# Kernel optimization log

Measured on AMD Instinct MI355X. Metric: run time of the kernel, lower is better.

Reference implementation:

```python
import jax, jax.numpy as jnp
from jax import lax
import numpy as np

B, S, IN = 8, 4096, 64
D, H, K = 512, 8, 3
TCN_CH = [256, 256, 512]
HD = D // H


def setup_inputs() -> dict:
    key = jax.random.key(0)
    ks = iter(jax.random.split(key, 64))
    def nrm(shape, s=0.02):
        return jax.random.normal(next(ks), shape, jnp.float32) * s
    inp = {"x": jax.random.normal(next(ks), (B, S, IN), jnp.float32)}
    inp["W_in"] = nrm((IN, D)); inp["b_in"] = jnp.zeros((D,), jnp.float32)
    chans = [D] + TCN_CH
    for i in range(3):
        cin, cout = chans[i], chans[i + 1]
        inp[f"c1w{i}"] = nrm((cout, cin, K), 0.01); inp[f"c1b{i}"] = jnp.zeros((cout,), jnp.float32)
        inp[f"c2w{i}"] = nrm((cout, cout, K), 0.01); inp[f"c2b{i}"] = jnp.zeros((cout,), jnp.float32)
        if cin != cout:  # downsample 1x1 conv (blocks 0 and 2)
            inp[f"dsw{i}"] = nrm((cout, cin, 1), 0.01); inp[f"dsb{i}"] = jnp.zeros((cout,), jnp.float32)
    inp["W_tcn"] = nrm((TCN_CH[-1], D)); inp["b_tcn"] = jnp.zeros((D,), jnp.float32)
    NL = 2  # attention layers, stacked on leading axis
    for n in ["Wq", "Wk", "Wv", "Wo"]:
        inp[n] = nrm((NL, D, D))
    for n in ["bq", "bk", "bv", "bo", "ln_b"]:
        inp[n] = jnp.zeros((NL, D), jnp.float32)
    inp["ln_g"] = jnp.ones((NL, D), jnp.float32)
    inp["W_out"] = nrm((D, 1)); inp["b_out"] = jnp.zeros((1,), jnp.float32)
    return inp


def _conv(x, w, b, dil, pad):
    # x: (B,C,L), w: (O,I,K)
    y = lax.conv_general_dilated(x, w, (1,), [(pad, pad)], rhs_dilation=(dil,),
                                 dimension_numbers=("NCH", "OIH", "NCH"))
    return y + b[None, :, None]


def _block(t, c1w, c1b, c2w, c2b, ds, dil):
    # TemporalConvBlock: symmetric padding (k-1)*dil on both convs, truncate to input length
    pad = (K - 1) * dil
    o = jax.nn.relu(_conv(t, c1w, c1b, dil, pad))   # length L + pad
    o = _conv(o, c2w, c2b, dil, pad)                # length L + 2*pad
    r = t if ds is None else _conv(t, ds[0], ds[1], 1, 0)
    return jax.nn.relu(o[:, :, : t.shape[2]] + r)


def _layernorm(x, g, b, eps=1e-5):
    mu = x.mean(-1, keepdims=True)
    var = ((x - mu) ** 2).mean(-1, keepdims=True)
    return (x - mu) * lax.rsqrt(var + eps) * g + b


def _forward(x, W_in, b_in, c1w0, c1b0, c2w0, c2b0, dsw0, dsb0,
             c1w1, c1b1, c2w1, c2b1, c1w2, c1b2, c2w2, c2b2, dsw2, dsb2,
             W_tcn, b_tcn, Wq, bq, Wk, bk, Wv, bv, Wo, bo, ln_g, ln_b, W_out, b_out):
    h = x @ W_in + b_in                              # (B,S,D)
    t = jnp.swapaxes(h, 1, 2)                        # (B,D,S)
    t = _block(t, c1w0, c1b0, c2w0, c2b0, (dsw0, dsb0), 1)
    t = _block(t, c1w1, c1b1, c2w1, c2b1, None, 2)
    t = _block(t, c1w2, c1b2, c2w2, c2b2, (dsw2, dsb2), 4)
    h = h + jnp.swapaxes(t, 1, 2) @ W_tcn + b_tcn
    # sinusoidal positional encoding
    pos = jnp.arange(S, dtype=jnp.float32)[:, None]
    div = jnp.exp(jnp.arange(0, D, 2, dtype=jnp.float32) * (-np.log(10000.0) / D))
    pe = jnp.stack([jnp.sin(pos * div), jnp.cos(pos * div)], axis=-1).reshape(S, D)
    h = h + pe[None]
    for l in range(Wq.shape[0]):
        res = h
        def heads(y):  # (B,S,D) -> (B,H,S,HD)
            return y.reshape(B, S, H, HD).transpose(0, 2, 1, 3)
        q = heads(h @ Wq[l] + bq[l])
        k = heads(h @ Wk[l] + bk[l])
        v = heads(h @ Wv[l] + bv[l])
        qf = jax.nn.elu(q) + 1.0
        kf = jax.nn.elu(k) + 1.0
        kv = jnp.einsum("bhnd,bhnm->bhdm", kf, v)            # (B,H,HD,HD)
        out = jnp.einsum("bhnd,bhdm->bhnm", qf, kv)          # (B,H,S,HD)
        norm = jnp.maximum(jnp.einsum("bhnd,bhd->bhn", qf, kf.sum(2)), 1e-6)
        out = out / norm[..., None]
        out = out.transpose(0, 2, 1, 3).reshape(B, S, D)
        h = _layernorm(res + out @ Wo[l] + bo[l], ln_g[l], ln_b[l])
    pooled = h.mean(1)                                       # (B,D)
    return (pooled @ W_out + b_out)[:, 0]                    # (B,)


def reference(x, W_in, b_in, c1w0, c1b0, c2w0, c2b0, dsw0, dsb0,
              c1w1, c1b1, c2w1, c2b1, c1w2, c1b2, c2w2, c2b2, dsw2, dsb2,
              W_tcn, b_tcn, Wq, bq, Wk, bk, Wv, bv, Wo, bo, ln_g, ln_b, W_out, b_out):
    return _forward(x, W_in, b_in, c1w0, c1b0, c2w0, c2b0, dsw0, dsb0,
                    c1w1, c1b1, c2w1, c2b1, c1w2, c1b2, c2w2, c2b2, dsw2, dsb2,
                    W_tcn, b_tcn, Wq, bq, Wk, bk, Wv, bv, Wo, bo, ln_g, ln_b, W_out, b_out)
```

## Files before the change

kernel.cpp:

```cpp
#include <hip/hip_runtime.h>

typedef unsigned short u16;
typedef unsigned int u32;
typedef short bhalf8 __attribute__((ext_vector_type(8)));
typedef float f32x4 __attribute__((ext_vector_type(4)));

#define S_LEN 4096
#define NSEG 30

__device__ __forceinline__ float b2f(u16 h){ return __uint_as_float(((u32)h) << 16); }
__device__ __forceinline__ u16 f2b(float f){
  u32 u = __float_as_uint(f);
  return (u16)((u + 0x7FFFu + ((u >> 16) & 1u)) >> 16);
}
__device__ __forceinline__ u32 cvtpk(float a, float b){
  u32 r; asm("v_cvt_pk_bf16_f32 %0, %1, %2" : "=v"(r) : "v"(a), "v"(b)); return r;
}
__device__ __forceinline__ void unp8(uint4 v, float* f){
  f[0]=__uint_as_float(v.x<<16); f[1]=__uint_as_float(v.x&0xffff0000u);
  f[2]=__uint_as_float(v.y<<16); f[3]=__uint_as_float(v.y&0xffff0000u);
  f[4]=__uint_as_float(v.z<<16); f[5]=__uint_as_float(v.z&0xffff0000u);
  f[6]=__uint_as_float(v.w<<16); f[7]=__uint_as_float(v.w&0xffff0000u);
}
__device__ __forceinline__ void unp4(uint2 v, float* f){
  f[0]=__uint_as_float(v.x<<16); f[1]=__uint_as_float(v.x&0xffff0000u);
  f[2]=__uint_as_float(v.y<<16); f[3]=__uint_as_float(v.y&0xffff0000u);
}

__device__ __forceinline__ size_t taddr(int r, int c, int C){
  return (size_t)(r >> 7) * ((size_t)C << 7) + (size_t)((c >> 5) << 12)
       + ((r & 127) << 5) + (c & 31);
}

__device__ __forceinline__ void gload16(const void* g, void* l){
  __builtin_amdgcn_global_load_lds(
      (__attribute__((address_space(1))) void*)(g),
      (__attribute__((address_space(3))) void*)(l), 16, 0, 0);
}

struct PrepArgs {
  const float* src[NSEG];
  int N[NSEG]; int K[NSEG]; int sn[NSEG]; int sk[NSEG]; unsigned off[NSEG];
};

__global__ __launch_bounds__(256) void prep_w(PrepArgs pa, u16* __restrict__ wb){
  int seg = blockIdx.y;
  int N = pa.N[seg], K = pa.K[seg];
  int ntk = (K + 31) >> 5;
  int tiles = ((N + 31) >> 5) * ntk;
  int tile = blockIdx.x;
  if (tile >= tiles) return;
  int n0 = (tile / ntk) << 5, k0 = (tile % ntk) << 5;
  const float* src = pa.src[seg];
  long sn = pa.sn[seg], sk = pa.sk[seg];
  u16* dst = wb + pa.off[seg];
  int lk = threadIdx.x & 31, ln = threadIdx.x >> 5;
  #pragma unroll
  for (int i = 0; i < 4; ++i){
    int n = n0 + ln + i*8, k = k0 + lk;
    if (n < N && k < K)
      dst[(size_t)n*K + k] = f2b(src[(long)n*sn + (long)k*sk]);
  }
}

__global__ __launch_bounds__(256) void pe_k(float* __restrict__ pe){
  int id = blockIdx.x*256 + threadIdx.x;
  int s = id >> 8, i = id & 255;
  float div = expf((float)i * (-2.0f * 9.210340371976184f / 512.0f));
  float a = (float)s * div;
  pe[(size_t)s*512 + 2*i]   = sinf(a);
  pe[(size_t)s*512 + 2*i+1] = cosf(a);
}

__global__ __launch_bounds__(256) void cvt_k(const float* __restrict__ x, u16* __restrict__ xb, int n){
  int id = blockIdx.x*256 + threadIdx.x;
  if (id < n){
    int r = id >> 6, c = id & 63;
    xb[taddr(r, c, 64)] = f2b(x[id]);
  }
}

template<int KTOT>
__global__ __launch_bounds__(512, 1) void gemm8_k(
    const u16* __restrict__ A, const u16* __restrict__ W,
    const float* __restrict__ bias, const float* __restrict__ bias2,
    const float* __restrict__ bias3,
    u16* __restrict__ out, const u16* __restrict__ resb,
    const float* __restrict__ peb,
    int N, int nN, int flags)
{
  constexpr int KT = KTOT >> 6;
  constexpr int IT = KT >> 1;
  __shared__ u16 As[2][16384];
  __shared__ u16 Bs[2][16384];
  const int tid = threadIdx.x;
  const int wave = tid >> 6, lane = tid & 63;
  const int wm = wave >> 2, wn = wave & 3;
  const int c0 = lane >> 4, fro = lane & 15;

  const int nwg = gridDim.x;
  const int lin = blockIdx.x;
  const int swz = (lin & 7) * (nwg >> 3) + (lin >> 3);
  const int mb = swz / nN, nb = swz - mb * nN;
  const int m0 = mb << 8, n0 = nb << 8;

  const f32x4 zf = {0.f,0.f,0.f,0.f};
  f32x4 acc[8][4];
  #pragma unroll
  for (int i=0;i<8;++i)
    #pragma unroll
    for (int j=0;j<4;++j) acc[i][j] = zf;

  bhalf8 af[2][2], bf[4][2];

  auto SA = [&](int t, int q){
    int s = (q << 9) + tid;
    int row = s >> 3, phys = s & 7;
    int lc = phys ^ (row & 7);
    int grow = m0 + row;
    int gcol = (t << 6) + (lc << 3);
    size_t ga = ((size_t)(grow >> 7) << 16) + (size_t)((gcol >> 5) << 12)
              + ((grow & 127) << 5) + (gcol & 31);
    gload16(A + ga, &As[t & 1][(q << 12) + (wave << 9)]);
  };
  auto SB = [&](int t, int j){
    int s = (j << 9) + tid;
    int row = s >> 3, phys = s & 7;
    int lc = phys ^ (row & 7);
    gload16(W + (size_t)(n0 + row) * KTOT + (t << 6) + (lc << 3),
            &Bs[t & 1][(j << 12) + (wave << 9)]);
  };
  auto LDB = [&](int t){
    #pragma unroll
    for (int nt=0;nt<4;++nt)
      #pragma unroll
      for (int ks=0;ks<2;++ks){
        int row = (wn << 6) + (nt << 4) + fro;
        int phys = ((ks << 2) + c0) ^ (row & 7);
        bf[nt][ks] = *(const bhalf8*)&Bs[t & 1][(row << 6) + (phys << 3)];
      }
  };
  auto LDA = [&](int t, int q){
    #pragma unroll
    for (int mtl=0;mtl<2;++mtl)
      #pragma unroll
      for (int ks=0;ks<2;++ks){
        int row = (q << 6) + (wm << 5) + (mtl << 4) + fro;
        int phys = ((ks << 2) + c0) ^ (row & 7);
        af[mtl][ks] = *(const bhalf8*)&As[t & 1][(row << 6) + (phys << 3)];
      }
  };
  auto BAR = [&]{
    __builtin_amdgcn_sched_barrier(0);
    __builtin_amdgcn_s_barrier();
    __builtin_amdgcn_sched_barrier(0);
  };
  auto MM = [&](int q){
    __builtin_amdgcn_s_setprio(1);
    #pragma unroll
    for (int mtl=0;mtl<2;++mtl)
      #pragma unroll
      for (int nt=0;nt<4;++nt){
        acc[(q<<1)+mtl][nt] = __builtin_amdgcn_mfma_f32_16x16x32_bf16(
            bf[nt][0], af[mtl][0], acc[(q<<1)+mtl][nt], 0, 0, 0);
        acc[(q<<1)+mtl][nt] = __builtin_amdgcn_mfma_f32_16x16x32_bf16(
            bf[nt][1], af[mtl][1], acc[(q<<1)+mtl][nt], 0, 0, 0);
      }
    __builtin_amdgcn_s_setprio(0);
  };

  #pragma unroll
  for (int x=0;x<4;++x){ SA(0,x); SB(0,x); }
  #pragma unroll
  for (int x=0;x<3;++x){ SA(1,x); SB(1,x); }
  asm volatile("s_waitcnt vmcnt(6)" ::: "memory");
  BAR();

  #pragma unroll
  for (int i=0;i<IT;++i){
    const int t0 = 2*i, t1 = 2*i+1, t2 = 2*i+2, t3 = 2*i+3;
    #pragma unroll
    for (int q=0;q<4;++q){
      if (q == 0) LDB(t0);
      LDA(t0, q);
      if (q == 0){ SA(t1,3); SB(t1,3); }
      else if (t2 < KT){ SA(t2,q-1); SB(t2,q-1); }
      BAR();
      MM(q);
      if (q == 3){
        if (t2 < KT) asm volatile("s_waitcnt vmcnt(6)" ::: "memory");
        else         asm volatile("s_waitcnt vmcnt(0)" ::: "memory");
      }
      BAR();
    }
    #pragma unroll
    for (int q=0;q<4;++q){
      if (q == 0) LDB(t1);
      LDA(t1, q);
      if (q == 0){ if (t2 < KT){ SA(t2,3); SB(t2,3); } }
      else if (t3 < KT){ SA(t3,q-1); SB(t3,q-1); }
      BAR();
      MM(q);
      if (q == 3 && (i + 1 < IT))
        asm volatile("s_waitcnt vmcnt(6)" ::: "memory");
      BAR();
    }
  }

  const int th = n0 >> 9;
  #pragma unroll
  for (int mt = 0; mt < 8; ++mt){
    const int row = m0 + ((mt >> 1) << 6) + (wm << 5) + ((mt & 1) << 4) + fro;
    const size_t prow = (size_t)(row & (S_LEN - 1)) * 512;
    #pragma unroll
    for (int nt = 0; nt < 4; ++nt){
      const int col = n0 + (wn << 6) + (nt << 4) + (c0 << 2);
      float v0 = acc[mt][nt][0], v1 = acc[mt][nt][1], v2 = acc[mt][nt][2], v3 = acc[mt][nt][3];
      if (flags & 32){
        const float* bp = (th == 0) ? bias : ((th == 1) ? bias2 : bias3);
        if (bp){ float4 b4 = *(const float4*)&bp[col & 511]; v0+=b4.x; v1+=b4.y; v2+=b4.z; v3+=b4.w; }
      } else {
        if (bias){ float4 b4 = *(const float4*)&bias[col]; v0+=b4.x; v1+=b4.y; v2+=b4.z; v3+=b4.w; }
      }
      if (flags & 4){
        uint2 rv = *(const uint2*)(resb + taddr(row, col, N));
        float rf[4]; unp4(rv, rf);
        v0 += rf[0]; v1 += rf[1]; v2 += rf[2]; v3 += rf[3];
      }
      if (flags & 8){
        float4 p4 = *(const float4*)&peb[prow + col];
        v0 += p4.x; v1 += p4.y; v2 += p4.z; v3 += p4.w;
      }
      if (flags & 1){
        v0 = fmaxf(v0, 0.f); v1 = fmaxf(v1, 0.f); v2 = fmaxf(v2, 0.f); v3 = fmaxf(v3, 0.f);
      }
      if ((flags & 2) && (!(flags & 32) || th < 2)){
        v0 = (v0 > 0.f) ? (v0 + 1.f) : __expf(v0);
        v1 = (v1 > 0.f) ? (v1 + 1.f) : __expf(v1);
        v2 = (v2 > 0.f) ? (v2 + 1.f) : __expf(v2);
        v3 = (v3 > 0.f) ? (v3 + 1.f) : __expf(v3);
      }
      uint2 pk; pk.x = cvtpk(v0, v1); pk.y = cvtpk(v2, v3);
      *(uint2*)(out + taddr(row, col, N)) = pk;
    }
  }
}

template<int NTAPS, int KS1, int KS2>
__global__ __launch_bounds__(256) void gemm_k(
    const u16* __restrict__ A, const u16* __restrict__ W,
    const u16* __restrict__ A2, const u16* __restrict__ W2,
    const float* __restrict__ bias, const float* __restrict__ bias2,
    const float* __restrict__ bias3,
    u16* __restrict__ out, const u16* __restrict__ resb,
    const float* __restrict__ peb, const float* __restrict__ den,
    int N, int CA, int CA2, int dil, int nN, int wbstride, int flags)
{
  constexpr bool MT   = (NTAPS == 3);
  constexpr int HALO  = MT ? 8 : 0;
  constexpr int AR    = MT ? 144 : 128;
  constexpr int DA    = MT ? ((KS2 > 0) ? 3 : 2) : 3;
  constexpr int DB    = 3;
  constexpr int K     = KS1 << 5;
  constexpr int K2    = KS2 << 5;
  constexpr int TOTAL = MT ? (3*KS1 + KS2) : (KS1 + KS2);
  __shared__ u16 As[DA][AR*32];
  __shared__ u16 Bs[DB][128*32];
  const int tid = threadIdx.x;
  const int wave = tid >> 6, lane = tid & 63;
  const int wm = wave >> 1, wn = wave & 1;

  const int nwg = gridDim.x;
  const int lin = blockIdx.x;
  const int swz = (lin & 7) * (nwg >> 3) + (lin >> 3);
  const int mb = swz / nN, nb = swz - mb * nN;
  const int m0 = mb << 7, n0 = nb << 7;
  const bool bnd = (m0 & (S_LEN - 1)) == 0;

  const u16* Ae = (flags & 16) ? (A + (((size_t)(n0 & 511) >> 5) << 12)) : A;

  const int lr4 = lane >> 2, lc4 = lane & 3;
  const int c0 = lane >> 4, fro = lane & 15;

  const f32x4 zf = {0.f, 0.f, 0.f, 0.f};
  const bhalf8 zb = {0,0,0,0,0,0,0,0};
  f32x4 acc[4][4];
  #pragma unroll
  for (int i=0;i<4;++i)
    #pragma unroll
    for (int j=0;j<4;++j) acc[i][j] = zf;

  const u16* Wb = W + (size_t)(m0 >> 12) * (size_t)wbstride;
  const size_t abase  = (size_t)mb * ((size_t)CA  << 7);
  const size_t abase2 = (size_t)mb * ((size_t)CA2 << 7);

  auto STAGE_A = [&](int kb, int ab){
    const size_t tb = abase + ((size_t)kb << 12);
    #pragma unroll
    for (int half = 0; half < 2; ++half){
      int mrow = (wave << 5) + (half << 4) + lr4;
      int i = mrow + HALO;
      int cg = lc4 ^ ((i >> 1) & 3);
      gload16(Ae + tb + mrow*32 + (cg << 3), &As[ab][(HALO + (wave << 5) + (half << 4)) * 32]);
    }
    if (MT && wave == 0 && lane < 32){
      int j = lr4;
      int cg = lc4 ^ ((j >> 1) & 3);
      size_t hb_ = (mb ? abase - ((size_t)CA << 7) : abase) + ((size_t)kb << 12) + (120 + j)*32;
      gload16(Ae + hb_ + (cg << 3), &As[ab][0]);
    }
  };
  auto STAGE_A2 = [&](int t2, int ab){
    const size_t tb = abase2 + ((size_t)t2 << 12);
    #pragma unroll
    for (int half = 0; half < 2; ++half){
      int mrow = (wave << 5) + (half << 4) + lr4;
      int i = mrow + HALO;
      int cg = lc4 ^ ((i >> 1) & 3);
      gload16(A2 + tb + mrow*32 + (cg << 3), &As[ab][(HALO + (wave << 5) + (half << 4)) * 32]);
    }
  };
  auto STAGE_B = [&](const u16* Wt, size_t kstride, int kb, int bb){
    #pragma unroll
    for (int half = 0; half < 2; ++half){
      int i = (wave << 5) + (half << 4) + lr4;
      int cg = lc4 ^ ((i >> 1) & 3);
      gload16(Wt + (size_t)(n0 + i) * kstride + (kb << 5) + (cg << 3),
              &Bs[bb][((wave << 5) + (half << 4)) * 32]);
    }
  };
  auto DO16 = [&](int ab, int bb, int sh, bool mask){
    bhalf8 af[4], bf[4];
    #pragma unroll
    for (int mt = 0; mt < 4; ++mt){
      int r8 = (wm << 6) + (mt << 4) + fro + HALO + sh;
      af[mt] = *(const bhalf8*)&As[ab][r8 * 32 + ((c0 ^ ((r8 >> 1) & 3)) << 3)];
    }
    if (MT && mask && bnd && wm == 0 && fro + sh < 0) af[0] = zb;
    #pragma unroll
    for (int nt = 0; nt < 4; ++nt){
      int rB = (wn << 6) + (nt << 4) + fro;
      bf[nt] = *(const bhalf8*)&Bs[bb][rB * 32 + ((c0 ^ ((rB >> 1) & 3)) << 3)];
    }
    #pragma unroll
    for (int mt = 0; mt < 4; ++mt)
      #pragma unroll
      for (int nt = 0; nt < 4; ++nt)
        acc[mt][nt] = __builtin_amdgcn_mfma_f32_16x16x32_bf16(bf[nt], af[mt], acc[mt][nt], 0, 0, 0);
  };

  if constexpr (!MT){
    auto STG = [&](int s){
      int b = s % 3;
      if (s < KS1){ STAGE_A(s, b); STAGE_B(Wb, (size_t)K, s, b); }
      else if (KS2 > 0){ STAGE_A2(s - KS1, b); STAGE_B(W2, (size_t)K2, s - KS1, b); }
    };
    STG(0);
    if constexpr (TOTAL > 1) STG(1);
    #pragma unroll
    for (int s = 0; s < TOTAL; ++s){
      if (s + 1 >= TOTAL) asm volatile("s_waitcnt vmcnt(0)" ::: "memory");
      else                asm volatile("s_waitcnt vmcnt(4)" ::: "memory");
      __builtin_amdgcn_sched_barrier(0);
      __builtin_amdgcn_s_barrier();
      __builtin_amdgcn_sched_barrier(0);
      if (s + 2 < TOTAL) STG(s + 2);
      DO16(s % 3, s % 3, 0, false);
    }
  } else {
    auto STG = [&](int s){
      if (s < 3*KS1){
        int kb = s / 3, tap = s % 3;
        if (tap == 0) STAGE_A(kb, kb % DA);
        STAGE_B(Wb + (size_t)tap * N * K, (size_t)K, kb, s % 3);
      } else if (KS2 > 0){
        int t2 = s - 3*KS1;
        STAGE_A2(t2, (KS1 + t2) % DA);
        STAGE_B(W2, (size_t)K2, t2, s % 3);
      }
    };
    STG(0);
    if constexpr (TOTAL > 1) STG(1);
    #pragma unroll
    for (int s = 0; s < TOTAL; ++s){
      if (s + 1 >= TOTAL) asm volatile("s_waitcnt vmcnt(0)" ::: "memory");
      else                asm volatile("s_waitcnt vmcnt(2)" ::: "memory");
      __builtin_amdgcn_sched_barrier(0);
      __builtin_amdgcn_s_barrier();
      __builtin_amdgcn_sched_barrier(0);
      if (s + 2 < TOTAL) STG(s + 2);
      if (s < 3*KS1) DO16((s/3) % DA, s % 3, ((s%3) - 2) * dil, true);
      else           DO16((KS1 + (s - 3*KS1)) % DA, s % 3, 0, false);
    }
  }

  const int mb_l = (wm << 6) + fro;
  const int cb_l = (wn << 6) + (c0 << 2);
  const int th = n0 >> 9;
  #pragma unroll
  for (int mt = 0; mt < 4; ++mt){
    const int row = m0 + mb_l + (mt << 4);
    const size_t prow = (size_t)(row & (S_LEN - 1)) * 512;
    #pragma unroll
    for (int nt = 0; nt < 4; ++nt){
      const int col = n0 + cb_l + (nt << 4);
      float v0 = acc[mt][nt][0], v1 = acc[mt][nt][1], v2 = acc[mt][nt][2], v3 = acc[mt][nt][3];
      if (flags & 32){
        const float* bp = (th == 0) ? bias : ((th == 1) ? bias2 : bias3);
        if (bp){ float4 b4 = *(const float4*)&bp[col & 511]; v0+=b4.x; v1+=b4.y; v2+=b4.z; v3+=b4.w; }
      } else {
        if (bias) { float4 b4 = *(const float4*)&bias[col];  v0+=b4.x; v1+=b4.y; v2+=b4.z; v3+=b4.w; }
        if (bias2){ float4 b4 = *(const float4*)&bias2[col]; v0+=b4.x; v1+=b4.y; v2+=b4.z; v3+=b4.w; }
      }
      if (flags & 4){
        uint2 rv = *(const uint2*)(resb + taddr(row, col, N));
        float rf[4]; unp4(rv, rf);
        v0 += rf[0]; v1 += rf[1]; v2 += rf[2]; v3 += rf[3];
      }
      if (flags & 8){
        float4 p4 = *(const float4*)&peb[prow + col];
        v0 += p4.x; v1 += p4.y; v2 += p4.z; v3 += p4.w;
      }
      if (flags & 16){
        float d = fmaxf(den[((size_t)row << 3) + (col >> 6)], 1e-6f);
        float rd = 1.0f / d;
        v0 *= rd; v1 *= rd; v2 *= rd; v3 *= rd;
      }
      if (flags & 1){
        v0 = fmaxf(v0, 0.f); v1 = fmaxf(v1, 0.f); v2 = fmaxf(v2, 0.f); v3 = fmaxf(v3, 0.f);
      }
      if ((flags & 2) && (!(flags & 32) || th < 2)){
        v0 = (v0 > 0.f) ? (v0 + 1.f) : __expf(v0);
        v1 = (v1 > 0.f) ? (v1 + 1.f) : __expf(v1);
        v2 = (v2 > 0.f) ? (v2 + 1.f) : __expf(v2);
        v3 = (v3 > 0.f) ? (v3 + 1.f) : __expf(v3);
      }
      uint2 pk; pk.x = cvtpk(v0, v1); pk.y = cvtpk(v2, v3);
      *(uint2*)(out + taddr(row, col, N)) = pk;
    }
  }
}

__global__ __launch_bounds__(256) void kv_partial(
    const u16* __restrict__ qkv,
    float* __restrict__ kvp, float* __restrict__ ksp)
{
  const int bh = blockIdx.x;
  const int b = bh >> 3, h = bh & 7;
  const int ch = blockIdx.y;
  const int t = threadIdx.x;
  __shared__ u16 kfs[16][64];
  __shared__ u16 vs[16][64];
  float acc[4][4] = {{0.f}};
  float ks[4] = {0.f,0.f,0.f,0.f};
  const int d0 = (t >> 4) << 2;
  const int c0 = (t & 15) << 2;
  const int lr = t >> 4, lc = (t & 15) << 2;
  const int rowbase = (b << 12) + (ch << 9);
  const int ck = 512 + (h << 6) + lc;
  const int cv = 1024 + (h << 6) + lc;
  for (int g = 0; g < 32; ++g){
    int r = rowbase + (g << 4) + lr;
    *(uint2*)&kfs[lr][lc] = *(const uint2*)(qkv + taddr(r, ck, 1536));
    *(uint2*)&vs[lr][lc]  = *(const uint2*)(qkv + taddr(r, cv, 1536));
    __syncthreads();
    #pragma unroll
    for (int i = 0; i < 16; ++i){
      float kv4[4], vv4[4];
      unp4(*(const uint2*)&kfs[i][d0], kv4);
      unp4(*(const uint2*)&vs[i][c0], vv4);
      #pragma unroll
      for (int j=0;j<4;++j)
        #pragma unroll
        for (int k2=0;k2<4;++k2) acc[j][k2] += kv4[j]*vv4[k2];
      if ((t & 15) == 0){
        #pragma unroll
        for (int j=0;j<4;++j) ks[j] += kv4[j];
      }
    }
    __syncthreads();
  }
  float* dst = kvp + ((size_t)(bh << 3) + ch) * 4096;
  #pragma unroll
  for (int j=0;j<4;++j)
    #pragma unroll
    for (int k2=0;k2<4;++k2) dst[(d0+j)*64 + (c0+k2)] = acc[j][k2];
  if ((t & 15) == 0){
    float* kd = ksp + ((size_t)(bh << 3) + ch) * 64;
    #pragma unroll
    for (int j=0;j<4;++j) kd[d0+j] = ks[j];
  }
}

__global__ __launch_bounds__(256) void kvred_k(
    const float* __restrict__ kvp, const float* __restrict__ ksp,
    float* __restrict__ kvf, float* __restrict__ ksf)
{
  int bh = blockIdx.x, t = threadIdx.x;
  for (int e = t; e < 4096; e += 256){
    float s = 0.f;
    #pragma unroll
    for (int ch = 0; ch < 8; ++ch) s += kvp[((size_t)(bh<<3)+ch)*4096 + e];
    kvf[(size_t)bh*4096 + e] = s;
  }
  if (t < 64){
    float s = 0.f;
    #pragma unroll
    for (int ch = 0; ch < 8; ++ch) s += ksp[((size_t)(bh<<3)+ch)*64 + t];
    ksf[bh*64 + t] = s;
  }
}

__global__ __launch_bounds__(256) void denpack_k(const u16* __restrict__ qkv,
    const float* __restrict__ ksf, float* __restrict__ den,
    const float* __restrict__ kvf, u16* __restrict__ wbd)
{
  int bid = blockIdx.x;
  if (bid < 1024){
    int id = bid*256 + threadIdx.x;
    int r = id >> 3, h = id & 7;
    int b = r >> 12;
    const float* ks = ksf + ((b<<3)+h)*64;
    float s = 0.f;
    for (int d = 0; d < 64; d += 8){
      uint4 vq = *(const uint4*)(qkv + taddr(r, (h << 6) + d, 1536));
      float f[8]; unp8(vq, f);
      #pragma unroll
      for (int j=0;j<8;++j) s += f[j]*ks[d+j];
    }
    den[id] = s;
  } else {
    int id = (bid - 1024)*256 + threadIdx.x;
    int b = id >> 16;
    int n = (id >> 7) & 511, j = id & 127;
    float v = 0.f;
    if ((j >> 6) == ((n >> 6) & 1))
      v = kvf[((size_t)((b<<3)+(n>>6)))*4096 + (j & 63)*64 + (n & 63)];
    wbd[id] = f2b(v);
  }
}

__global__ __launch_bounds__(256) void ln_k(const u16* __restrict__ in,
    const float* __restrict__ g, const float* __restrict__ beta, u16* __restrict__ out)
{
  int wave = threadIdx.x >> 6, lane = threadIdx.x & 63;
  int row = blockIdx.x*4 + wave;
  size_t ad = taddr(row, lane*8, 512);
  uint4 pv = *(const uint4*)(in + ad);
  float f[8]; unp8(pv, f);
  float s = 0.f, ss = 0.f;
  #pragma unroll
  for (int i=0;i<8;++i){ s += f[i]; ss += f[i]*f[i]; }
  for (int m=1;m<64;m<<=1){ s += __shfl_xor(s,m); ss += __shfl_xor(ss,m); }
  float mean = s * (1.f/512.f);
  float var = ss * (1.f/512.f) - mean*mean;
  float rstd = rsqrtf(fmaxf(var, 0.f) + 1e-5f);
  u16 o[8];
  #pragma unroll
  for (int i=0;i<8;++i){
    int c = lane*8 + i;
    o[i] = f2b((f[i]-mean)*rstd*g[c] + beta[c]);
  }
  *(uint4*)(out + ad) = *(uint4*)o;
}

__global__ __launch_bounds__(256) void pool1_k(const u16* __restrict__ hb,
    const float* __restrict__ wout, const float* __restrict__ g,
    const float* __restrict__ beta, float* __restrict__ part)
{
  int b = blockIdx.x >> 6, ch = blockIdx.x & 63;
  int t = threadIdx.x;
  __shared__ float ws[512];
  __shared__ float red[256];
  __shared__ float S2[2];
  float a0 = 0.f, a1 = 0.f;
  for (int i = t; i < 512; i += 256){
    float w = wout[i];
    float gw = w * g[i];
    ws[i] = gw;
    a0 += gw;
    a1 += w * beta[i];
  }
  red[t] = a0; __syncthreads();
  for (int k2=128;k2;k2>>=1){ if (t<k2) red[t]+=red[t+k2]; __syncthreads(); }
  if (!t) S2[0] = red[0];
  __syncthreads();
  red[t] = a1; __syncthreads();
  for (int k2=128;k2;k2>>=1){ if (t<k2) red[t]+=red[t+k2]; __syncthreads(); }
  if (!t) S2[1] = red[0];
  __syncthreads();
  const float Sgw = S2[0], Sbw = S2[1];

  int r = (b << 12) + (ch << 6) + (t >> 2);
  int c0 = (t & 3) << 7;
  float sd = 0.f, s1 = 0.f, s2 = 0.f;
  for (int i = 0; i < 128; i += 8){
    uint4 v = *(const uint4*)(hb + taddr(r, c0 + i, 512));
    float f[8]; unp8(v, f);
    #pragma unroll
    for (int j=0;j<8;++j){ float x = f[j]; sd += x*ws[c0+i+j]; s1 += x; s2 += x*x; }
  }
  sd += __shfl_xor(sd,1); s1 += __shfl_xor(s1,1); s2 += __shfl_xor(s2,1);
  sd += __shfl_xor(sd,2); s1 += __shfl_xor(s1,2); s2 += __shfl_xor(s2,2);
  float mean = s1 * (1.f/512.f);
  float var  = s2 * (1.f/512.f) - mean*mean;
  float rstd = rsqrtf(fmaxf(var, 0.f) + 1e-5f);
  float rowv = rstd * (sd - mean * Sgw) + Sbw;
  red[t] = ((t & 3) == 0) ? rowv : 0.f;
  __syncthreads();
  for (int k2=128;k2;k2>>=1){ if (t<k2) red[t]+=red[t+k2]; __syncthreads(); }
  if (!t) part[blockIdx.x] = red[0];
}

__global__ __launch_bounds__(64) void pool2_k(const float* __restrict__ part,
    const float* __restrict__ bout, float* __restrict__ out)
{
  int b = blockIdx.x, t = threadIdx.x;
  float s = part[(b << 6) + t];
  for (int m=1;m<64;m<<=1) s += __shfl_xor(s,m);
  if (!t) out[b] = s * (1.f/4096.f) + bout[0];
}

extern "C" void kernel_launch(void* const* d_in, const int* in_sizes, int n_in,
                              void* d_out, int out_size, void* d_ws, size_t ws_size,
                              hipStream_t stream)
{
  (void)in_sizes; (void)n_in; (void)out_size; (void)ws_size;
  const float* x    = (const float*)d_in[0];
  const float* W_in = (const float*)d_in[1];
  const float* b_in = (const float*)d_in[2];
  const float* c1w0 = (const float*)d_in[3];
  const float* c1b0 = (const float*)d_in[4];
  const float* c2w0 = (const float*)d_in[5];
  const float* c2b0 = (const float*)d_in[6];
  const float* dsw0 = (const float*)d_in[7];
  const float* dsb0 = (const float*)d_in[8];
  const float* c1w1 = (const float*)d_in[9];
  const float* c1b1 = (const float*)d_in[10];
  const float* c2w1 = (const float*)d_in[11];
  const float* c2b1 = (const float*)d_in[12];
  const float* c1w2 = (const float*)d_in[13];
  const float* c1b2 = (const float*)d_in[14];
  const float* c2w2 = (const float*)d_in[15];
  const float* c2b2 = (const float*)d_in[16];
  const float* dsw2 = (const float*)d_in[17];
  const float* dsb2 = (const float*)d_in[18];
  const float* W_tcn= (const float*)d_in[19];
  const float* b_tcn= (const float*)d_in[20];
  const float* Wq   = (const float*)d_in[21];
  const float* Wk   = (const float*)d_in[22];
  const float* Wv   = (const float*)d_in[23];
  const float* Wo   = (const float*)d_in[24];
  const float* bq   = (const float*)d_in[25];
  const float* bk   = (const float*)d_in[26];
  const float* bv   = (const float*)d_in[27];
  const float* bo   = (const float*)d_in[28];
  const float* lnb  = (const float*)d_in[29];
  const float* lng  = (const float*)d_in[30];
  const float* W_out= (const float*)d_in[31];
  const float* b_out= (const float*)d_in[32];

  char* base = (char*)d_ws;
  size_t off = 0;
  auto alloc = [&](size_t bytes) -> void* {
    void* p = base + off;
    off += (bytes + 255) & ~(size_t)255;
    return p;
  };
  u16* WB   = (u16*)alloc(4816896ull*2);
  u16* wbd  = (u16*)alloc(8ull*512*128*2);
  float* peb= (float*)alloc(4096ull*512*4);
  float* den= (float*)alloc(32768ull*8*4);
  float* kvp= (float*)alloc(512ull*4096*4);
  float* ksp= (float*)alloc(512ull*64*4);
  float* kvf= (float*)alloc(64ull*4096*4);
  float* ksf= (float*)alloc(64ull*64*4);
  float* part=(float*)alloc(512*4);
  u16* hb   = (u16*)alloc(32768ull*512*2);
  char* qkvR= (char*)alloc(32768ull*1536*2);
  u16* atto = (u16*)alloc(32768ull*512*2);

  u16* qkvb = (u16*)qkvR;
  u16* xb   = (u16*)(qkvR);
  u16* t1b  = (u16*)(qkvR + 4194304);
  u16* t2b  = (u16*)(qkvR + 20971520);
  u16* t3b  = (u16*)(qkvR + 37748736);
  u16* o1b  = atto;

  unsigned wo_ = 0;
  auto wseg = [&](unsigned e){ unsigned o = wo_; wo_ += e; return o; };
  unsigned oWin  = wseg(512*64);
  unsigned oC1w0 = wseg(3*256*512);
  unsigned oC2w0 = wseg(3*256*256);
  unsigned oDs0  = wseg(256*512);
  unsigned oC1w1 = wseg(3*256*256);
  unsigned oC2w1 = wseg(3*256*256);
  unsigned oC1w2 = wseg(3*512*256);
  unsigned oC2w2 = wseg(3*512*512);
  unsigned oDs2  = wseg(512*256);
  unsigned oWtcn = wseg(512*512);
  unsigned oQKV  = wseg(2*1536*512);
  unsigned oWo   = wseg(2*512*512);

  PrepArgs pa;
  int si = 0;
  auto seg = [&](const float* s, int N, int K, int sn, int sk, unsigned o){
    pa.src[si]=s; pa.N[si]=N; pa.K[si]=K; pa.sn[si]=sn; pa.sk[si]=sk; pa.off[si]=o; ++si;
  };
  seg(W_in, 512, 64, 1, 512, oWin);
  for (int t=0;t<3;++t) seg(c1w0 + t, 256, 512, 1536, 3, oC1w0 + t*131072);
  for (int t=0;t<3;++t) seg(c2w0 + t, 256, 256,  768, 3, oC2w0 + t*65536);
  seg(dsw0, 256, 512, 512, 1, oDs0);
  for (int t=0;t<3;++t) seg(c1w1 + t, 256, 256,  768, 3, oC1w1 + t*65536);
  for (int t=0;t<3;++t) seg(c2w1 + t, 256, 256,  768, 3, oC2w1 + t*65536);
  for (int t=0;t<3;++t) seg(c1w2 + t, 512, 256,  768, 3, oC1w2 + t*131072);
  for (int t=0;t<3;++t) seg(c2w2 + t, 512, 512, 1536, 3, oC2w2 + t*262144);
  seg(dsw2, 512, 256, 256, 1, oDs2);
  seg(W_tcn, 512, 512, 1, 512, oWtcn);
  for (int l=0;l<2;++l){
    seg(Wq + l*262144, 512, 512, 1, 512, oQKV + l*786432 + 0);
    seg(Wk + l*262144, 512, 512, 1, 512, oQKV + l*786432 + 262144);
    seg(Wv + l*262144, 512, 512, 1, 512, oQKV + l*786432 + 524288);
  }
  for (int l=0;l<2;++l) seg(Wo + l*262144, 512, 512, 1, 512, oWo + l*262144);

  prep_w<<<dim3(256, NSEG), 256, 0, stream>>>(pa, WB);
  pe_k<<<4096, 256, 0, stream>>>(peb);
  cvt_k<<<8192, 256, 0, stream>>>(x, xb, 32768*64);

  const int RELU=1, ELU1=2, RES=4, PE=8, DIV=16, QKV=32;
  auto gemm = [&](const u16* A, const u16* W, const u16* A2, const u16* W2,
                  const float* b1, const float* b2, const float* b3,
                  u16* out, const u16* resb,
                  int K, int K2, int N, int CA, int CA2, int ntaps,
                  int dil, int wbs, int flags){
    int nN = N >> 7;
    dim3 grid(256 * nN);
    if (ntaps == 3){
      if (K == 512 && K2 == 0)
        gemm_k<3,16,0><<<grid, 256, 0, stream>>>(A, W, A2, W2, b1, b2, b3, out, resb,
                                                 peb, den, N, CA, CA2, dil, nN, wbs, flags);
      else if (K == 256 && K2 == 512)
        gemm_k<3,8,16><<<grid, 256, 0, stream>>>(A, W, A2, W2, b1, b2, b3, out, resb,
                                                 peb, den, N, CA, CA2, dil, nN, wbs, flags);
      else if (K == 256 && K2 == 0)
        gemm_k<3,8,0><<<grid, 256, 0, stream>>>(A, W, A2, W2, b1, b2, b3, out, resb,
                                                peb, den, N, CA, CA2, dil, nN, wbs, flags);
      else
        gemm_k<3,16,8><<<grid, 256, 0, stream>>>(A, W, A2, W2, b1, b2, b3, out, resb,
                                                 peb, den, N, CA, CA2, dil, nN, wbs, flags);
    } else {
      if (K == 64)
        gemm_k<1,2,0><<<grid, 256, 0, stream>>>(A, W, A2, W2, b1, b2, b3, out, resb,
                                                peb, den, N, CA, CA2, dil, nN, wbs, flags);
      else
        gemm_k<1,4,0><<<grid, 256, 0, stream>>>(A, W, A2, W2, b1, b2, b3, out, resb,
                                                peb, den, N, CA, CA2, dil, nN, wbs, flags);
    }
  };
  auto gemm8 = [&](const u16* A, const u16* W, const float* b1, const float* b2,
                   const float* b3, u16* out, const u16* resb, int N, int flags){
    int nN = N >> 8;
    gemm8_k<512><<<dim3(128 * nN), 512, 0, stream>>>(A, W, b1, b2, b3, out, resb,
                                                     peb, N, nN, flags);
  };

  gemm(xb, WB + oWin, nullptr, nullptr, b_in, nullptr, nullptr, hb, nullptr,
       64, 0, 512, 64, 0, 1, 1, 0, 0);
  gemm(hb,  WB + oC1w0, nullptr, nullptr, c1b0, nullptr, nullptr, o1b, nullptr,
       512, 0, 256, 512, 0, 3, 1, 0, RELU);
  gemm(o1b, WB + oC2w0, hb, WB + oDs0, c2b0, dsb0, nullptr, t1b, nullptr,
       256, 512, 256, 256, 512, 3, 1, 0, RELU);
  gemm(t1b, WB + oC1w1, nullptr, nullptr, c1b1, nullptr, nullptr, o1b, nullptr,
       256, 0, 256, 256, 0, 3, 2, 0, RELU);
  gemm(o1b, WB + oC2w1, nullptr, nullptr, c2b1, nullptr, nullptr, t2b, t1b,
       256, 0, 256, 256, 0, 3, 2, 0, RELU|RES);
  gemm(t2b, WB + oC1w2, nullptr, nullptr, c1b2, nullptr, nullptr, o1b, nullptr,
       256, 0, 512, 256, 0, 3, 4, 0, RELU);
  gemm(o1b, WB + oC2w2, t2b, WB + oDs2, c2b2, dsb2, nullptr, t3b, nullptr,
       512, 256, 512, 512, 256, 3, 4, 0, RELU);
  gemm8(t3b, WB + oWtcn, b_tcn, nullptr, nullptr, hb, hb, 512, RES|PE);

  for (int l = 0; l < 2; ++l){
    gemm8(hb, WB + oQKV + l*786432, bq + l*512, bk + l*512, bv + l*512,
          qkvb, nullptr, 1536, ELU1|QKV);
    kv_partial<<<dim3(64, 8), 256, 0, stream>>>(qkvb, kvp, ksp);
    kvred_k<<<64, 256, 0, stream>>>(kvp, ksp, kvf, ksf);
    denpack_k<<<3072, 256, 0, stream>>>(qkvb, ksf, den, kvf, wbd);
    gemm(qkvb, wbd, nullptr, nullptr, nullptr, nullptr, nullptr, atto, nullptr,
         128, 0, 512, 1536, 0, 1, 1, 512*128, DIV);
    gemm8(atto, WB + oWo + l*262144, bo + l*512, nullptr, nullptr, hb, hb, 512, RES);
    if (l == 0)
      ln_k<<<8192, 256, 0, stream>>>(hb, lng, lnb, hb);
  }

  pool1_k<<<512, 256, 0, stream>>>(hb, W_out, lng + 512, lnb + 512, part);
  pool2_k<<<8, 64, 0, stream>>>(part, b_out, (float*)d_out);
}
```

Before: 763.3 us.

## Fold per-batch KV state into Wo to merge attention output and projection GEMMs

Instead of computing attn = (q/den)·KV with a block-diagonal GEMM and then multiplying by Wo, the code precomputes per-batch folded weights KV·Wo (512x512 per batch) and normalizes q in place by its denominator. A single gemm8 then takes the normalized q columns directly (CA=1536, per-batch weight stride) and applies bias and residual. This removes one full GEMM launch and the intermediate attention-output buffer round trip. In exchange it adds a per-batch 512x512 weight product computed with scalar FMAs and an extra bf16 rounding of the normalized q.

New measurement: 855.9 us. 1.12x slower.

```diff
diff --git a/kernel.cpp b/kernel.cpp
--- a/kernel.cpp
+++ b/kernel.cpp
@@ -87,7 +87,7 @@
     const float* __restrict__ bias3,
     u16* __restrict__ out, const u16* __restrict__ resb,
     const float* __restrict__ peb,
-    int N, int nN, int flags)
+    int N, int nN, int CA, int wbs, int flags)
 {
   constexpr int KT = KTOT >> 6;
   constexpr int IT = KT >> 1;
@@ -104,6 +104,8 @@
   const int mb = swz / nN, nb = swz - mb * nN;
   const int m0 = mb << 8, n0 = nb << 8;
 
+  const u16* Wp = W + (size_t)(m0 >> 12) * (size_t)wbs;
+
   const f32x4 zf = {0.f,0.f,0.f,0.f};
   f32x4 acc[8][4];
   #pragma unroll
@@ -119,7 +121,7 @@
     int lc = phys ^ (row & 7);
     int grow = m0 + row;
     int gcol = (t << 6) + (lc << 3);
-    size_t ga = ((size_t)(grow >> 7) << 16) + (size_t)((gcol >> 5) << 12)
+    size_t ga = (size_t)(grow >> 7) * ((size_t)CA << 7) + (size_t)((gcol >> 5) << 12)
               + ((grow & 127) << 5) + (gcol & 31);
     gload16(A + ga, &As[t & 1][(q << 12) + (wave << 9)]);
   };
@@ -127,7 +129,7 @@
     int s = (j << 9) + tid;
     int row = s >> 3, phys = s & 7;
     int lc = phys ^ (row & 7);
-    gload16(W + (size_t)(n0 + row) * KTOT + (t << 6) + (lc << 3),
+    gload16(Wp + (size_t)(n0 + row) * KTOT + (t << 6) + (lc << 3),
             &Bs[t & 1][(j << 12) + (wave << 9)]);
   };
   auto LDB = [&](int t){
@@ -253,7 +255,7 @@
     const float* __restrict__ bias, const float* __restrict__ bias2,
     const float* __restrict__ bias3,
     u16* __restrict__ out, const u16* __restrict__ resb,
-    const float* __restrict__ peb, const float* __restrict__ den,
+    const float* __restrict__ peb,
     int N, int CA, int CA2, int dil, int nN, int wbstride, int flags)
 {
   constexpr bool MT   = (NTAPS == 3);
@@ -277,8 +279,6 @@
   const int m0 = mb << 7, n0 = nb << 7;
   const bool bnd = (m0 & (S_LEN - 1)) == 0;
 
-  const u16* Ae = (flags & 16) ? (A + (((size_t)(n0 & 511) >> 5) << 12)) : A;
-
   const int lr4 = lane >> 2, lc4 = lane & 3;
   const int c0 = lane >> 4, fro = lane & 15;
 
@@ -301,13 +301,13 @@
       int mrow = (wave << 5) + (half << 4) + lr4;
       int i = mrow + HALO;
       int cg = lc4 ^ ((i >> 1) & 3);
-      gload16(Ae + tb + mrow*32 + (cg << 3), &As[ab][(HALO + (wave << 5) + (half << 4)) * 32]);
+      gload16(A + tb + mrow*32 + (cg << 3), &As[ab][(HALO + (wave << 5) + (half << 4)) * 32]);
     }
     if (MT && wave == 0 && lane < 32){
       int j = lr4;
       int cg = lc4 ^ ((j >> 1) & 3);
       size_t hb_ = (mb ? abase - ((size_t)CA << 7) : abase) + ((size_t)kb << 12) + (120 + j)*32;
-      gload16(Ae + hb_ + (cg << 3), &As[ab][0]);
+      gload16(A + hb_ + (cg << 3), &As[ab][0]);
     }
   };
   auto STAGE_A2 = [&](int t2, int ab){
@@ -420,11 +420,6 @@
       if (flags & 8){
         float4 p4 = *(const float4*)&peb[prow + col];
         v0 += p4.x; v1 += p4.y; v2 += p4.z; v3 += p4.w;
-      }
-      if (flags & 16){
-        float d = fmaxf(den[((size_t)row << 3) + (col >> 6)], 1e-6f);
-        float rd = 1.0f / d;
-        v0 *= rd; v1 *= rd; v2 *= rd; v3 *= rd;
       }
       if (flags & 1){
         v0 = fmaxf(v0, 0.f); v1 = fmaxf(v1, 0.f); v2 = fmaxf(v2, 0.f); v3 = fmaxf(v3, 0.f);
@@ -511,9 +506,9 @@
   }
 }
 
-__global__ __launch_bounds__(256) void denpack_k(const u16* __restrict__ qkv,
-    const float* __restrict__ ksf, float* __restrict__ den,
-    const float* __restrict__ kvf, u16* __restrict__ wbd)
+__global__ __launch_bounds__(256) void denwf_k(u16* __restrict__ qkv,
+    const float* __restrict__ ksf, const float* __restrict__ kvf,
+    const u16* __restrict__ wo, u16* __restrict__ wft)
 {
   int bid = blockIdx.x;
   if (bid < 1024){
@@ -521,22 +516,43 @@
     int r = id >> 3, h = id & 7;
     int b = r >> 12;
     const float* ks = ksf + ((b<<3)+h)*64;
+    float f[64];
     float s = 0.f;
-    for (int d = 0; d < 64; d += 8){
-      uint4 vq = *(const uint4*)(qkv + taddr(r, (h << 6) + d, 1536));
-      float f[8]; unp8(vq, f);
+    #pragma unroll
+    for (int i=0;i<8;++i){
+      uint4 vq = *(const uint4*)(qkv + taddr(r, (h<<6) + i*8, 1536));
+      float g[8]; unp8(vq, g);
       #pragma unroll
-      for (int j=0;j<8;++j) s += f[j]*ks[d+j];
-    }
-    den[id] = s;
+      for (int j=0;j<8;++j){ f[i*8+j] = g[j]; s += g[j]*ks[i*8+j]; }
+    }
+    float rd = 1.0f / fmaxf(s, 1e-6f);
+    #pragma unroll
+    for (int i=0;i<8;++i){
+      uint4 o;
+      o.x = cvtpk(f[i*8+0]*rd, f[i*8+1]*rd);
+      o.y = cvtpk(f[i*8+2]*rd, f[i*8+3]*rd);
+      o.z = cvtpk(f[i*8+4]*rd, f[i*8+5]*rd);
+      o.w = cvtpk(f[i*8+6]*rd, f[i*8+7]*rd);
+      *(uint4*)(qkv + taddr(r, (h<<6) + i*8, 1536)) = o;
+    }
   } else {
     int id = (bid - 1024)*256 + threadIdx.x;
-    int b = id >> 16;
-    int n = (id >> 7) & 511, j = id & 127;
-    float v = 0.f;
-    if ((j >> 6) == ((n >> 6) & 1))
-      v = kvf[((size_t)((b<<3)+(n>>6)))*4096 + (j & 63)*64 + (n & 63)];
-    wbd[id] = f2b(v);
+    int b = id >> 18;
+    int n = (id >> 9) & 511, k = id & 511;
+    int h = k >> 6, d = k & 63;
+    const float* kvr = kvf + ((size_t)((b<<3)+h))*4096 + (d<<6);
+    const u16* wor = wo + (size_t)n*512 + (h<<6);
+    float s = 0.f;
+    #pragma unroll
+    for (int m=0;m<64;m+=8){
+      uint4 wv = *(const uint4*)(wor + m);
+      float wf8[8]; unp8(wv, wf8);
+      float4 k0 = *(const float4*)(kvr+m);
+      float4 k1 = *(const float4*)(kvr+m+4);
+      s += k0.x*wf8[0]+k0.y*wf8[1]+k0.z*wf8[2]+k0.w*wf8[3]
+         + k1.x*wf8[4]+k1.y*wf8[5]+k1.z*wf8[6]+k1.w*wf8[7];
+    }
+    wft[id] = f2b(s);
   }
 }
 
@@ -668,9 +684,8 @@
     return p;
   };
   u16* WB   = (u16*)alloc(4816896ull*2);
-  u16* wbd  = (u16*)alloc(8ull*512*128*2);
+  u16* wft  = (u16*)alloc(8ull*512*512*2);
   float* peb= (float*)alloc(4096ull*512*4);
-  float* den= (float*)alloc(32768ull*8*4);
   float* kvp= (float*)alloc(512ull*4096*4);
   float* ksp= (float*)alloc(512ull*64*4);
   float* kvf= (float*)alloc(64ull*4096*4);
@@ -728,7 +743,7 @@
   pe_k<<<4096, 256, 0, stream>>>(peb);
   cvt_k<<<8192, 256, 0, stream>>>(x, xb, 32768*64);
 
-  const int RELU=1, ELU1=2, RES=4, PE=8, DIV=16, QKV=32;
+  const int RELU=1, ELU1=2, RES=4, PE=8, QKV=32;
   auto gemm = [&](const u16* A, const u16* W, const u16* A2, const u16* W2,
                   const float* b1, const float* b2, const float* b3,
                   u16* out, const u16* resb,
@@ -739,30 +754,27 @@
     if (ntaps == 3){
       if (K == 512 && K2 == 0)
         gemm_k<3,16,0><<<grid, 256, 0, stream>>>(A, W, A2, W2, b1, b2, b3, out, resb,
-                                                 peb, den, N, CA, CA2, dil, nN, wbs, flags);
+                                                 peb, N, CA, CA2, dil, nN, wbs, flags);
       else if (K == 256 && K2 == 512)
         gemm_k<3,8,16><<<grid, 256, 0, stream>>>(A, W, A2, W2, b1, b2, b3, out, resb,
-                                                 peb, den, N, CA, CA2, dil, nN, wbs, flags);
+                                                 peb, N, CA, CA2, dil, nN, wbs, flags);
       else if (K == 256 && K2 == 0)
         gemm_k<3,8,0><<<grid, 256, 0, stream>>>(A, W, A2, W2, b1, b2, b3, out, resb,
-                                                peb, den, N, CA, CA2, dil, nN, wbs, flags);
+                                                peb, N, CA, CA2, dil, nN, wbs, flags);
       else
         gemm_k<3,16,8><<<grid, 256, 0, stream>>>(A, W, A2, W2, b1, b2, b3, out, resb,
-                                                 peb, den, N, CA, CA2, dil, nN, wbs, flags);
+                                                 peb, N, CA, CA2, dil, nN, wbs, flags);
     } else {
-      if (K == 64)
-        gemm_k<1,2,0><<<grid, 256, 0, stream>>>(A, W, A2, W2, b1, b2, b3, out, resb,
-                                                peb, den, N, CA, CA2, dil, nN, wbs, flags);
-      else
-        gemm_k<1,4,0><<<grid, 256, 0, stream>>>(A, W, A2, W2, b1, b2, b3, out, resb,
-                                                peb, den, N, CA, CA2, dil, nN, wbs, flags);
+      gemm_k<1,2,0><<<grid, 256, 0, stream>>>(A, W, A2, W2, b1, b2, b3, out, resb,
+                                              peb, N, CA, CA2, dil, nN, wbs, flags);
     }
   };
   auto gemm8 = [&](const u16* A, const u16* W, const float* b1, const float* b2,
-                   const float* b3, u16* out, const u16* resb, int N, int flags){
+                   const float* b3, u16* out, const u16* resb, int N, int CA,
+                   int wbs, int flags){
     int nN = N >> 8;
     gemm8_k<512><<<dim3(128 * nN), 512, 0, stream>>>(A, W, b1, b2, b3, out, resb,
-                                                     peb, N, nN, flags);
+                                                     peb, N, nN, CA, wbs, flags);
   };
 
   gemm(xb, WB + oWin, nullptr, nullptr, b_in, nullptr, nullptr, hb, nullptr,
@@ -779,17 +791,15 @@
        256, 0, 512, 256, 0, 3, 4, 0, RELU);
   gemm(o1b, WB + oC2w2, t2b, WB + oDs2, c2b2, dsb2, nullptr, t3b, nullptr,
        512, 256, 512, 512, 256, 3, 4, 0, RELU);
-  gemm8(t3b, WB + oWtcn, b_tcn, nullptr, nullptr, hb, hb, 512, RES|PE);
+  gemm8(t3b, WB + oWtcn, b_tcn, nullptr, nullptr, hb, hb, 512, 512, 0, RES|PE);
 
   for (int l = 0; l < 2; ++l){
     gemm8(hb, WB + oQKV + l*786432, bq + l*512, bk + l*512, bv + l*512,
-          qkvb, nullptr, 1536, ELU1|QKV);
+          qkvb, nullptr, 1536, 512, 0, ELU1|QKV);
     kv_partial<<<dim3(64, 8), 256, 0, stream>>>(qkvb, kvp, ksp);
     kvred_k<<<64, 256, 0, stream>>>(kvp, ksp, kvf, ksf);
-    denpack_k<<<3072, 256, 0, stream>>>(qkvb, ksf, den, kvf, wbd);
-    gemm(qkvb, wbd, nullptr, nullptr, nullptr, nullptr, nullptr, atto, nullptr,
-         128, 0, 512, 1536, 0, 1, 1, 512*128, DIV);
-    gemm8(atto, WB + oWo + l*262144, bo + l*512, nullptr, nullptr, hb, hb, 512, RES);
+    denwf_k<<<9216, 256, 0, stream>>>(qkvb, ksf, kvf, WB + oWo + l*262144, wft);
+    gemm8(qkvb, wft, bo + l*512, nullptr, nullptr, hb, hb, 512, 1536, 262144, RES);
     if (l == 0)
       ln_k<<<8192, 256, 0, stream>>>(hb, lng, lnb, hb);
   }
```
